# Optimization experiments

Hardware: AMD Instinct MI355X
Metric: run time of the kernel (lower is better)

Reference implementation:

```python
import jax, jax.numpy as jnp
import numpy as np

OUT_SIZE = 7
SAMPLE_NUM = 2
FEATMAP_STRIDES = (4, 8, 16, 32)
FINEST_SCALE = 56.0
IMG_H, IMG_W = 800, 1216
NUM_ROIS = 1024


def _bilinear_gather(feat, b, ys, xs):
    """Bilinearly sample feat[b] at grid (ys x xs).
    feat: [B,C,H,W]; b: [K] int32; ys,xs: [K,S] float sample coords.
    Returns [K,S,S,C].
    """
    H, W = feat.shape[2], feat.shape[3]
    valid_y = (ys >= -1.0) & (ys <= H)
    valid_x = (xs >= -1.0) & (xs <= W)
    y = jnp.clip(ys, 0.0)
    x = jnp.clip(xs, 0.0)
    yl = jnp.floor(y).astype(jnp.int32)
    xl = jnp.floor(x).astype(jnp.int32)
    # edge handling as in the CUDA roi_align kernel
    y = jnp.where(yl >= H - 1, jnp.asarray(H - 1, y.dtype), y)
    x = jnp.where(xl >= W - 1, jnp.asarray(W - 1, x.dtype), x)
    yl = jnp.minimum(yl, H - 1)
    xl = jnp.minimum(xl, W - 1)
    yh = jnp.minimum(yl + 1, H - 1)
    xh = jnp.minimum(xl + 1, W - 1)
    ly = y - yl.astype(y.dtype)
    lx = x - xl.astype(x.dtype)
    hy = 1.0 - ly
    hx = 1.0 - lx
    bb = b[:, None, None]                      # [K,1,1]
    Yl, Yh = yl[:, :, None], yh[:, :, None]    # [K,S,1]
    Xl, Xh = xl[:, None, :], xh[:, None, :]    # [K,1,S]

    def g(yi, xi):
        return feat[bb, :, yi, xi]             # [K,S,S,C]

    w_ll = (hy[:, :, None] * hx[:, None, :])[..., None]
    w_lh = (hy[:, :, None] * lx[:, None, :])[..., None]
    w_hl = (ly[:, :, None] * hx[:, None, :])[..., None]
    w_hh = (ly[:, :, None] * lx[:, None, :])[..., None]
    out = g(Yl, Xl) * w_ll
    out = out + g(Yl, Xh) * w_lh
    out = out + g(Yh, Xl) * w_hl
    out = out + g(Yh, Xh) * w_hh
    valid = (valid_y[:, :, None] & valid_x[:, None, :])[..., None]
    return jnp.where(valid, out, 0.0)


def roi_align(feat, rois, spatial_scale, out_size=OUT_SIZE, sr=SAMPLE_NUM):
    """RoIAlign (aligned=False, mmdet-v1 style). feat [B,C,H,W], rois [K,5].
    Returns [K,C,out,out].
    """
    K = rois.shape[0]
    C = feat.shape[1]
    b = rois[:, 0].astype(jnp.int32)
    x1 = rois[:, 1] * spatial_scale
    y1 = rois[:, 2] * spatial_scale
    x2 = rois[:, 3] * spatial_scale
    y2 = rois[:, 4] * spatial_scale
    roi_w = jnp.maximum(x2 - x1, 1.0)
    roi_h = jnp.maximum(y2 - y1, 1.0)
    S = out_size * sr
    grid = jnp.arange(S, dtype=feat.dtype) + 0.5  # [S]
    ys = y1[:, None] + grid[None, :] * (roi_h / S)[:, None]  # [K,S]
    xs = x1[:, None] + grid[None, :] * (roi_w / S)[:, None]
    v = _bilinear_gather(feat, b, ys, xs)                    # [K,S,S,C]
    v = v.reshape(K, out_size, sr, out_size, sr, C).mean(axis=(2, 4))
    return jnp.transpose(v, (0, 3, 1, 2))                    # [K,C,out,out]


def setup_inputs() -> dict:
    key = jax.random.key(0)
    ks = jax.random.split(key, 10)
    shapes = [(2, 256, 200, 304), (2, 256, 100, 152), (2, 256, 50, 76), (2, 256, 25, 38)]
    feats = [jax.random.normal(ks[i], s, dtype=jnp.float32) for i, s in enumerate(shapes)]
    K = NUM_ROIS
    b = jax.random.randint(ks[4], (K,), 0, 2).astype(jnp.float32)
    cx = jax.random.uniform(ks[5], (K,)) * IMG_W
    cy = jax.random.uniform(ks[6], (K,)) * IMG_H
    # box sizes spanning 8..512 px so all 4 FPN levels are exercised
    w = 2.0 ** (jax.random.uniform(ks[7], (K,)) * 6.0 + 3.0)
    h = 2.0 ** (jax.random.uniform(ks[8], (K,)) * 6.0 + 3.0)
    x1 = jnp.clip(cx - w * 0.5, 0.0, IMG_W - 1.0)
    y1 = jnp.clip(cy - h * 0.5, 0.0, IMG_H - 1.0)
    x2 = jnp.clip(cx + w * 0.5, 0.0, IMG_W - 1.0)
    y2 = jnp.clip(cy + h * 0.5, 0.0, IMG_H - 1.0)
    x2 = jnp.maximum(x2, x1)
    y2 = jnp.maximum(y2, y1)
    rois = jnp.stack([b, x1, y1, x2, y2], axis=-1)
    return {"feat0": feats[0], "feat1": feats[1], "feat2": feats[2], "feat3": feats[3], "rois": rois}


def reference(feat0, feat1, feat2, feat3, rois):
    feats = [feat0, feat1, feat2, feat3]
    num_levels = len(feats)
    # map_roi_levels
    scale = jnp.sqrt((rois[:, 3] - rois[:, 1] + 1.0) * (rois[:, 4] - rois[:, 2] + 1.0))
    lvls = jnp.floor(jnp.log2(scale / FINEST_SCALE + 1e-6))
    lvls = jnp.clip(lvls, 0, num_levels - 1).astype(jnp.int32)
    out = jnp.zeros((rois.shape[0], feat0.shape[1], OUT_SIZE, OUT_SIZE), dtype=feat0.dtype)
    for i in range(num_levels):
        rf = roi_align(feats[i], rois, 1.0 / FEATMAP_STRIDES[i])
        out = jnp.where((lvls == i)[:, None, None, None], rf, out)
    return out
```

## Files before the change

### kernel.cpp

```cpp
#include <hip/hip_runtime.h>

typedef unsigned int uint32;

namespace {
constexpr int CCH = 256;
constexpr int OUT = 7;
constexpr int S   = 14;
constexpr int NUM_ROIS = 1024;

constexpr int H0 = 200, W0 = 304;
constexpr int H1 = 100, W1 = 152;
constexpr int H2 = 50,  W2 = 76;
constexpr int H3 = 25,  W3 = 38;

constexpr int HW0 = H0 * W0;
constexpr int HW1 = H1 * W1;
constexpr int HW2 = H2 * W2;
constexpr int HW3 = H3 * W3;

constexpr size_t US0 = (size_t)2 * HW0 * CCH;
constexpr size_t US1 = (size_t)2 * HW1 * CCH;
constexpr size_t US2 = (size_t)2 * HW2 * CCH;
constexpr size_t US3 = (size_t)2 * HW3 * CCH;

constexpr int TT0 = (HW0 + 63) / 64;
constexpr int TT1 = (HW1 + 63) / 64;
constexpr int TT2 = (HW2 + 63) / 64;
constexpr int TT3 = (HW3 + 63) / 64;
constexpr int GG0 = 4 * TT0;
constexpr int GG1 = 4 * TT1;
constexpr int GG2 = 4 * TT2;
constexpr int GG3 = 4 * TT3;

constexpr int RWORDS = 257;
}

__device__ __forceinline__ unsigned short f2bf(float f) {
    uint32 u = __float_as_uint(f);
    u += 0x7fffu + ((u >> 16) & 1u);
    return (unsigned short)(u >> 16);
}
__device__ __forceinline__ float blo(uint32 u) { return __uint_as_float(u << 16); }
__device__ __forceinline__ float bhi(uint32 u) { return __uint_as_float(u & 0xffff0000u); }

__global__ __launch_bounds__(256) void transpose_gll(
    const float* __restrict__ f0, const float* __restrict__ f1,
    const float* __restrict__ f2, const float* __restrict__ f3,
    unsigned short* __restrict__ o0, unsigned short* __restrict__ o1,
    unsigned short* __restrict__ o2, unsigned short* __restrict__ o3)
{
    __shared__ uint32 lds[32 * RWORDS];
    int r = blockIdx.x;
    const float* in; unsigned short* op; int HW, TT;
    if (r < GG0)               {                  in = f0; op = o0; HW = HW0; TT = TT0; }
    else if (r < GG0+GG1)      { r -= GG0;        in = f1; op = o1; HW = HW1; TT = TT1; }
    else if (r < GG0+GG1+GG2)  { r -= GG0+GG1;    in = f2; op = o2; HW = HW2; TT = TT2; }
    else                       { r -= GG0+GG1+GG2; in = f3; op = o3; HW = HW3; TT = TT3; }
    const int b    = r / (2 * TT);
    const int rest = r - b * 2 * TT;
    const int half = rest / TT;
    const int tile = rest - half * TT;
    const int hw0  = tile * 64;

    const int t = threadIdx.x;
    const int l = t & 63;
    const int w = t >> 6;

    const float* src = in + (size_t)(b * CCH + half * 128) * HW;
    const bool fast = ((HW & 3) == 0) && (hw0 + 64 <= HW);

    if (fast) {
        #pragma unroll
        for (int j = 0; j < 8; ++j) {
            const int reg = w * 8 + j;
            const int c   = 4 * reg + (l >> 4);
            const float* g = src + (size_t)c * HW + hw0 + (l & 15) * 4;
            __builtin_amdgcn_global_load_lds(
                (const __attribute__((address_space(1))) void*)g,
                (__attribute__((address_space(3))) void*)&lds[reg * RWORDS],
                16, 0, 0);
        }
        asm volatile("s_waitcnt vmcnt(0)" ::: "memory");
        __syncthreads();
    } else {
        #pragma unroll 1
        for (int j = 0; j < 8; ++j) {
            const int reg = w * 8 + j;
            const int c   = 4 * reg + (l >> 4);
            const int hwb = hw0 + (l & 15) * 4;
            #pragma unroll
            for (int i = 0; i < 4; ++i) {
                const int hw = hwb + i;
                float v = 0.0f;
                if (hw < HW) v = src[(size_t)c * HW + hw];
                lds[reg * RWORDS + l * 4 + i] = __float_as_uint(v);
            }
        }
        __syncthreads();
    }

    const int n    = min(64, HW - hw0);
    const int hw   = t >> 2;
    const int csub = t & 3;
    if (hw < n) {
        uint32 outw[16];
        #pragma unroll
        for (int m = 0; m < 16; ++m) {
            const int c0 = csub * 32 + 2 * m;
            const int c1 = c0 + 1;
            const uint32 b0 = lds[(c0 >> 2) * RWORDS + (c0 & 3) * 64 + hw];
            const uint32 b1 = lds[(c1 >> 2) * RWORDS + (c1 & 3) * 64 + hw];
            outw[m] = (uint32)f2bf(__uint_as_float(b0))
                    | ((uint32)f2bf(__uint_as_float(b1)) << 16);
        }
        unsigned short* ob =
            op + ((size_t)b * HW + hw0 + hw) * CCH + half * 128 + csub * 32;
        *reinterpret_cast<uint4*>(ob +  0) = make_uint4(outw[0],  outw[1],  outw[2],  outw[3]);
        *reinterpret_cast<uint4*>(ob +  8) = make_uint4(outw[4],  outw[5],  outw[6],  outw[7]);
        *reinterpret_cast<uint4*>(ob + 16) = make_uint4(outw[8],  outw[9],  outw[10], outw[11]);
        *reinterpret_cast<uint4*>(ob + 24) = make_uint4(outw[12], outw[13], outw[14], outw[15]);
    }
}

__global__ __launch_bounds__(256) void roi_gather_bf16(
    const unsigned short* __restrict__ w0, const unsigned short* __restrict__ w1,
    const unsigned short* __restrict__ w2, const unsigned short* __restrict__ w3,
    const float* __restrict__ rois, float* __restrict__ out)
{
    const int k = blockIdx.x;
    const int t = threadIdx.x;

    __shared__ float s_wlo[2][S];
    __shared__ float s_whi[2][S];
    __shared__ int   s_olo[2][S];
    __shared__ int   s_ohi[2][S];
    __shared__ __align__(16) float s_out[25 * 260];

    const float rb  = rois[k*5+0];
    const float rx1 = rois[k*5+1];
    const float ry1 = rois[k*5+2];
    const float rx2 = rois[k*5+3];
    const float ry2 = rois[k*5+4];

    const float sc = sqrtf((rx2 - rx1 + 1.0f) * (ry2 - ry1 + 1.0f));
    int lvl = (int)floorf(log2f(sc * (1.0f/56.0f) + 1e-6f));
    lvl = lvl < 0 ? 0 : (lvl > 3 ? 3 : lvl);

    const unsigned short* fp; int H, W; float sp;
    if (lvl == 0)      { fp = w0; H = H0; W = W0; sp = 0.25f;    }
    else if (lvl == 1) { fp = w1; H = H1; W = W1; sp = 0.125f;   }
    else if (lvl == 2) { fp = w2; H = H2; W = W2; sp = 0.0625f;  }
    else               { fp = w3; H = H3; W = W3; sp = 0.03125f; }

    if (t < 2*S) {
        const int axis = (t >= S) ? 1 : 0;
        const int i = axis ? (t - S) : t;
        const float lo = (axis ? rx1 : ry1) * sp;
        const float hi = (axis ? rx2 : ry2) * sp;
        const int dim  = axis ? W : H;
        const float len = fmaxf(hi - lo, 1.0f);
        const float bin = len * (1.0f / (float)S);
        const float v = lo + ((float)i + 0.5f) * bin;
        const bool valid = (v >= -1.0f) && (v <= (float)dim);
        float vc = fmaxf(v, 0.0f);
        int l = (int)floorf(vc);
        if (l >= dim - 1) { vc = (float)(dim - 1); l = dim - 1; }
        const int h = min(l + 1, dim - 1);
        const float frac = vc - (float)l;
        float wlo = 1.0f - frac;
        float whi = frac;
        if (!valid) { wlo = 0.0f; whi = 0.0f; }
        const int mul = axis ? 64 : W * 64;
        s_wlo[axis][i] = wlo;
        s_whi[axis][i] = whi;
        s_olo[axis][i] = l * mul;
        s_ohi[axis][i] = h * mul;
    }
    __syncthreads();

    const int b = (int)rb;
    const int lane = t & 63;
    const int wv   = t >> 6;
    const uint2* __restrict__ base =
        reinterpret_cast<const uint2*>(fp) + (size_t)b * H * W * 64 + lane;
    float* __restrict__ ob = out + (size_t)k * CCH * (OUT * OUT);

    #pragma unroll
    for (int hf = 0; hf < 2; ++hf) {
        const int bb = hf ? 25 : 0;
        const int ne = hf ? 24 : 25;

        for (int bl = wv; bl < ne; bl += 4) {
            const int bin = bb + bl;
            const int oh = bin / 7;
            const int ow = bin - oh * 7;
            const int sy0 = oh * 2, sx0 = ow * 2;
            float a0 = 0.f, a1 = 0.f, a2 = 0.f, a3 = 0.f;
            #pragma unroll
            for (int dy = 0; dy < 2; ++dy) {
                const float hy = s_wlo[0][sy0 + dy];
                const float ly = s_whi[0][sy0 + dy];
                const int oyl = s_olo[0][sy0 + dy];
                const int oyh = s_ohi[0][sy0 + dy];
                #pragma unroll
                for (int dx = 0; dx < 2; ++dx) {
                    const float hx = s_wlo[1][sx0 + dx];
                    const float lx = s_whi[1][sx0 + dx];
                    const int oxl = s_olo[1][sx0 + dx];
                    const int oxh = s_ohi[1][sx0 + dx];
                    const uint2 qll = base[oyl + oxl];
                    const uint2 qlh = base[oyl + oxh];
                    const uint2 qhl = base[oyh + oxl];
                    const uint2 qhh = base[oyh + oxh];
                    const float wll = hy * hx, wlh = hy * lx;
                    const float whl = ly * hx, whh = ly * lx;
                    a0 += wll*blo(qll.x) + wlh*blo(qlh.x) + whl*blo(qhl.x) + whh*blo(qhh.x);
                    a1 += wll*bhi(qll.x) + wlh*bhi(qlh.x) + whl*bhi(qhl.x) + whh*bhi(qhh.x);
                    a2 += wll*blo(qll.y) + wlh*blo(qlh.y) + whl*blo(qhl.y) + whh*blo(qhh.y);
                    a3 += wll*bhi(qll.y) + wlh*bhi(qlh.y) + whl*bhi(qhl.y) + whh*bhi(qhh.y);
                }
            }
            float4 res = make_float4(a0*0.25f, a1*0.25f, a2*0.25f, a3*0.25f);
            *reinterpret_cast<float4*>(&s_out[bl * 260 + 4 * lane]) = res;
        }
        __syncthreads();

        #pragma unroll 1
        for (int j = 0; j < ne; ++j) {
            const int f = t + j * 256;
            const int c = f / ne;
            const int bl = f - c * ne;
            ob[c * (OUT*OUT) + bb + bl] = s_out[bl * 260 + c];
        }
        __syncthreads();
    }
}

__global__ __launch_bounds__(256) void roi_extract_direct(
    const float* __restrict__ f0, const float* __restrict__ f1,
    const float* __restrict__ f2, const float* __restrict__ f3,
    const float* __restrict__ rois, float* __restrict__ out)
{
    const int k = blockIdx.x;
    const int t = threadIdx.x;

    __shared__ float s_wlo[2][S];
    __shared__ float s_whi[2][S];
    __shared__ int   s_olo[2][S];
    __shared__ int   s_ohi[2][S];

    const float rb  = rois[k*5+0];
    const float rx1 = rois[k*5+1];
    const float ry1 = rois[k*5+2];
    const float rx2 = rois[k*5+3];
    const float ry2 = rois[k*5+4];

    const float sc = sqrtf((rx2 - rx1 + 1.0f) * (ry2 - ry1 + 1.0f));
    int lvl = (int)floorf(log2f(sc * (1.0f/56.0f) + 1e-6f));
    lvl = lvl < 0 ? 0 : (lvl > 3 ? 3 : lvl);

    const float* fp; int H, W; float sp;
    if (lvl == 0)      { fp = f0; H = H0; W = W0; sp = 0.25f;    }
    else if (lvl == 1) { fp = f1; H = H1; W = W1; sp = 0.125f;   }
    else if (lvl == 2) { fp = f2; H = H2; W = W2; sp = 0.0625f;  }
    else               { fp = f3; H = H3; W = W3; sp = 0.03125f; }

    if (t < 2*S) {
        const int axis = (t >= S) ? 1 : 0;
        const int i = axis ? (t - S) : t;
        const float lo = (axis ? rx1 : ry1) * sp;
        const float hi = (axis ? rx2 : ry2) * sp;
        const int dim  = axis ? W : H;
        const float len = fmaxf(hi - lo, 1.0f);
        const float bin = len * (1.0f / (float)S);
        const float v = lo + ((float)i + 0.5f) * bin;
        const bool valid = (v >= -1.0f) && (v <= (float)dim);
        float vc = fmaxf(v, 0.0f);
        int l = (int)floorf(vc);
        if (l >= dim - 1) { vc = (float)(dim - 1); l = dim - 1; }
        const int h = min(l + 1, dim - 1);
        const float frac = vc - (float)l;
        float wlo = 1.0f - frac;
        float whi = frac;
        if (!valid) { wlo = 0.0f; whi = 0.0f; }
        const int mul = axis ? 1 : W;
        s_wlo[axis][i] = wlo;
        s_whi[axis][i] = whi;
        s_olo[axis][i] = l * mul;
        s_ohi[axis][i] = h * mul;
    }
    __syncthreads();

    const int b = (int)rb;
    const float* __restrict__ base = fp + (size_t)(b * CCH + t) * (size_t)(H * W);
    float* __restrict__ obase = out + ((size_t)k * CCH + t) * (OUT * OUT);

    for (int oh = 0; oh < OUT; ++oh) {
        const int sy0 = oh * 2;
        const float hy0 = s_wlo[0][sy0],   ly0 = s_whi[0][sy0];
        const float hy1 = s_wlo[0][sy0+1], ly1 = s_whi[0][sy0+1];
        const int oyl0 = s_olo[0][sy0],   oyh0 = s_ohi[0][sy0];
        const int oyl1 = s_olo[0][sy0+1], oyh1 = s_ohi[0][sy0+1];
        #pragma unroll
        for (int ow = 0; ow < OUT; ++ow) {
            float acc = 0.0f;
            #pragma unroll
            for (int dx = 0; dx < 2; ++dx) {
                const int sx = ow * 2 + dx;
                const float hx = s_wlo[1][sx];
                const float lx = s_whi[1][sx];
                const int oxl = s_olo[1][sx];
                const int oxh = s_ohi[1][sx];
                acc += hy0 * (hx * base[oyl0 + oxl] + lx * base[oyl0 + oxh])
                     + ly0 * (hx * base[oyh0 + oxl] + lx * base[oyh0 + oxh])
                     + hy1 * (hx * base[oyl1 + oxl] + lx * base[oyl1 + oxh])
                     + ly1 * (hx * base[oyh1 + oxl] + lx * base[oyh1 + oxh]);
            }
            obase[oh * OUT + ow] = acc * 0.25f;
        }
    }
}

extern "C" void kernel_launch(void* const* d_in, const int* in_sizes, int n_in,
                              void* d_out, int out_size, void* d_ws, size_t ws_size,
                              hipStream_t stream) {
    const float* f0   = (const float*)d_in[0];
    const float* f1   = (const float*)d_in[1];
    const float* f2   = (const float*)d_in[2];
    const float* f3   = (const float*)d_in[3];
    const float* rois = (const float*)d_in[4];
    float* out = (float*)d_out;

    const size_t need_bytes = (US0 + US1 + US2 + US3) * sizeof(unsigned short);
    if (ws_size >= need_bytes) {
        unsigned short* ws0 = (unsigned short*)d_ws;
        unsigned short* ws1 = ws0 + US0;
        unsigned short* ws2 = ws1 + US1;
        unsigned short* ws3 = ws2 + US2;
        transpose_gll<<<GG0 + GG1 + GG2 + GG3, 256, 0, stream>>>(
            f0, f1, f2, f3, ws0, ws1, ws2, ws3);
        roi_gather_bf16<<<NUM_ROIS, 256, 0, stream>>>(ws0, ws1, ws2, ws3, rois, out);
    } else {
        roi_extract_direct<<<NUM_ROIS, 256, 0, stream>>>(f0, f1, f2, f3, rois, out);
    }
}
```

Baseline: 98.88 us.

## Convert to bf16 in registers before LDS transpose, halving shared memory

The transpose kernel now loads fp32 features into registers with float4 loads instead of using direct global-to-LDS async loads. It converts to bf16 and packs channel pairs before writing a smaller padded LDS tile (64x65 words instead of 32x257). Readback becomes contiguous 16-word row reads. The smaller LDS footprint and a launch bound of 8 blocks per CU are meant to raise occupancy and cut LDS traffic, but the change drops the async LDS load path and adds register pressure.

```diff
diff --git a/kernel.cpp b/kernel.cpp
--- a/kernel.cpp
+++ b/kernel.cpp
@@ -32,7 +32,7 @@
 constexpr int GG2 = 4 * TT2;
 constexpr int GG3 = 4 * TT3;
 
-constexpr int RWORDS = 257;
+constexpr int LSTR = 65;
 }
 
 __device__ __forceinline__ unsigned short f2bf(float f) {
@@ -43,13 +43,13 @@
 __device__ __forceinline__ float blo(uint32 u) { return __uint_as_float(u << 16); }
 __device__ __forceinline__ float bhi(uint32 u) { return __uint_as_float(u & 0xffff0000u); }
 
-__global__ __launch_bounds__(256) void transpose_gll(
+__global__ __launch_bounds__(256, 8) void transpose_hi(
     const float* __restrict__ f0, const float* __restrict__ f1,
     const float* __restrict__ f2, const float* __restrict__ f3,
     unsigned short* __restrict__ o0, unsigned short* __restrict__ o1,
     unsigned short* __restrict__ o2, unsigned short* __restrict__ o3)
 {
-    __shared__ uint32 lds[32 * RWORDS];
+    __shared__ uint32 lds[64 * LSTR];
     int r = blockIdx.x;
     const float* in; unsigned short* op; int HW, TT;
     if (r < GG0)               {                  in = f0; op = o0; HW = HW0; TT = TT0; }
@@ -62,63 +62,72 @@
     const int tile = rest - half * TT;
     const int hw0  = tile * 64;
 
-    const int t = threadIdx.x;
-    const int l = t & 63;
-    const int w = t >> 6;
-
-    const float* src = in + (size_t)(b * CCH + half * 128) * HW;
+    const int t  = threadIdx.x;
+    const int hq = t & 7;
+    const int cq = t >> 3;
+
+    const float* src = in + (size_t)(b * CCH + half * 128 + 4 * cq) * HW;
     const bool fast = ((HW & 3) == 0) && (hw0 + 64 <= HW);
 
+    float4 v[8];
     if (fast) {
+        const float* base = src + hw0 + 8 * hq;
         #pragma unroll
-        for (int j = 0; j < 8; ++j) {
-            const int reg = w * 8 + j;
-            const int c   = 4 * reg + (l >> 4);
-            const float* g = src + (size_t)c * HW + hw0 + (l & 15) * 4;
-            __builtin_amdgcn_global_load_lds(
-                (const __attribute__((address_space(1))) void*)g,
-                (__attribute__((address_space(3))) void*)&lds[reg * RWORDS],
-                16, 0, 0);
-        }
-        asm volatile("s_waitcnt vmcnt(0)" ::: "memory");
-        __syncthreads();
+        for (int j = 0; j < 4; ++j) {
+            #pragma unroll
+            for (int h = 0; h < 2; ++h)
+                v[j * 2 + h] = *reinterpret_cast<const float4*>(
+                    base + (size_t)j * HW + 4 * h);
+        }
     } else {
-        #pragma unroll 1
-        for (int j = 0; j < 8; ++j) {
-            const int reg = w * 8 + j;
-            const int c   = 4 * reg + (l >> 4);
-            const int hwb = hw0 + (l & 15) * 4;
-            #pragma unroll
-            for (int i = 0; i < 4; ++i) {
-                const int hw = hwb + i;
-                float v = 0.0f;
-                if (hw < HW) v = src[(size_t)c * HW + hw];
-                lds[reg * RWORDS + l * 4 + i] = __float_as_uint(v);
+        #pragma unroll
+        for (int j = 0; j < 4; ++j) {
+            #pragma unroll
+            for (int h = 0; h < 2; ++h) {
+                float4 a = make_float4(0.f, 0.f, 0.f, 0.f);
+                const int hwb = hw0 + 8 * hq + 4 * h;
+                const float* p = src + (size_t)j * HW + hwb;
+                if (hwb + 0 < HW) a.x = p[0];
+                if (hwb + 1 < HW) a.y = p[1];
+                if (hwb + 2 < HW) a.z = p[2];
+                if (hwb + 3 < HW) a.w = p[3];
+                v[j * 2 + h] = a;
             }
         }
-        __syncthreads();
-    }
-
-    const int n    = min(64, HW - hw0);
-    const int hw   = t >> 2;
-    const int csub = t & 3;
-    if (hw < n) {
-        uint32 outw[16];
+    }
+
+    #pragma unroll
+    for (int p = 0; p < 2; ++p) {
         #pragma unroll
-        for (int m = 0; m < 16; ++m) {
-            const int c0 = csub * 32 + 2 * m;
-            const int c1 = c0 + 1;
-            const uint32 b0 = lds[(c0 >> 2) * RWORDS + (c0 & 3) * 64 + hw];
-            const uint32 b1 = lds[(c1 >> 2) * RWORDS + (c1 & 3) * 64 + hw];
-            outw[m] = (uint32)f2bf(__uint_as_float(b0))
-                    | ((uint32)f2bf(__uint_as_float(b1)) << 16);
-        }
-        unsigned short* ob =
-            op + ((size_t)b * HW + hw0 + hw) * CCH + half * 128 + csub * 32;
-        *reinterpret_cast<uint4*>(ob +  0) = make_uint4(outw[0],  outw[1],  outw[2],  outw[3]);
-        *reinterpret_cast<uint4*>(ob +  8) = make_uint4(outw[4],  outw[5],  outw[6],  outw[7]);
-        *reinterpret_cast<uint4*>(ob + 16) = make_uint4(outw[8],  outw[9],  outw[10], outw[11]);
-        *reinterpret_cast<uint4*>(ob + 24) = make_uint4(outw[12], outw[13], outw[14], outw[15]);
+        for (int h = 0; h < 2; ++h) {
+            const float4 lo = v[(2 * p) * 2 + h];
+            const float4 hi = v[(2 * p + 1) * 2 + h];
+            const int row = 8 * hq + 4 * h;
+            const int col = 2 * cq + p;
+            lds[(row + 0) * LSTR + col] = (uint32)f2bf(lo.x) | ((uint32)f2bf(hi.x) << 16);
+            lds[(row + 1) * LSTR + col] = (uint32)f2bf(lo.y) | ((uint32)f2bf(hi.y) << 16);
+            lds[(row + 2) * LSTR + col] = (uint32)f2bf(lo.z) | ((uint32)f2bf(hi.z) << 16);
+            lds[(row + 3) * LSTR + col] = (uint32)f2bf(lo.w) | ((uint32)f2bf(hi.w) << 16);
+        }
+    }
+    __syncthreads();
+
+    {
+        const int row = t >> 2;
+        const int qd  = t & 3;
+        const int n   = min(64, HW - hw0);
+        if (row < n) {
+            uint32 wv[16];
+            #pragma unroll
+            for (int m = 0; m < 16; ++m)
+                wv[m] = lds[row * LSTR + 16 * qd + m];
+            unsigned short* ob =
+                op + ((size_t)b * HW + hw0 + row) * CCH + half * 128 + qd * 32;
+            *reinterpret_cast<uint4*>(ob +  0) = make_uint4(wv[0],  wv[1],  wv[2],  wv[3]);
+            *reinterpret_cast<uint4*>(ob +  8) = make_uint4(wv[4],  wv[5],  wv[6],  wv[7]);
+            *reinterpret_cast<uint4*>(ob + 16) = make_uint4(wv[8],  wv[9],  wv[10], wv[11]);
+            *reinterpret_cast<uint4*>(ob + 24) = make_uint4(wv[12], wv[13], wv[14], wv[15]);
+        }
     }
 }
 
@@ -337,7 +346,7 @@
         unsigned short* ws1 = ws0 + US0;
         unsigned short* ws2 = ws1 + US1;
         unsigned short* ws3 = ws2 + US2;
-        transpose_gll<<<GG0 + GG1 + GG2 + GG3, 256, 0, stream>>>(
+        transpose_hi<<<GG0 + GG1 + GG2 + GG3, 256, 0, stream>>>(
             f0, f1, f2, f3, ws0, ws1, ws2, ws3);
         roi_gather_bf16<<<NUM_ROIS, 256, 0, stream>>>(ws0, ws1, ws2, ws3, rois, out);
     } else {
```

After: 97.07 us. No clear change (-1.8%).
